# Kernel tuning notes

Measured on AMD Instinct MI355X. Metric: run time of the kernel, lower is better.

Reference implementation:

```python
import jax, jax.numpy as jnp
import numpy as np

N_USERS = 100000
M_ITEMS = 50000
N = N_USERS + M_ITEMS
D = 64
NNZ = 4800000
N_LAYERS = 3


def spmm(idx, val, x):
    # sparse COO (idx[0]=rows, idx[1]=cols) @ dense x : gather-scale-scatter
    rows, cols = idx[0], idx[1]
    return jax.ops.segment_sum(val[:, None] * x[cols], rows, num_segments=N)


def propagate(idx, val, emb0):
    # LightGCN propagation: mean over layer-0..n_layers embeddings
    embs = [emb0]
    e = emb0
    for _ in range(N_LAYERS):
        e = spmm(idx, val, e)
        embs.append(e)
    return jnp.mean(jnp.stack(embs, axis=1), axis=1)  # [N, D]


def setup_inputs() -> dict:
    key = jax.random.key(0)
    ks = jax.random.split(key, 10)
    return {
        "emb_im": 0.1 * jax.random.normal(ks[0], (N, D), jnp.float32),
        "emb_q": 0.1 * jax.random.normal(ks[1], (N, D), jnp.float32),
        "emb_p": 0.1 * jax.random.normal(ks[2], (N, D), jnp.float32),
        "g_im_idx": jax.random.randint(ks[3], (2, NNZ), 0, N, jnp.int32),
        "g_im_val": jax.random.uniform(ks[4], (NNZ,), jnp.float32) / 32.0,
        "g_q_idx": jax.random.randint(ks[5], (2, NNZ), 0, N, jnp.int32),
        "g_q_val": jax.random.uniform(ks[6], (NNZ,), jnp.float32) / 32.0,
        "g_p_idx": jax.random.randint(ks[7], (2, NNZ), 0, N, jnp.int32),
        "g_p_val": jax.random.uniform(ks[8], (NNZ,), jnp.float32) / 32.0,
        "add_weight": jnp.ones((3,), jnp.float32),
    }


def reference(emb_im, emb_q, emb_p, g_im_idx, g_im_val, g_q_idx, g_q_val,
              g_p_idx, g_p_val, add_weight):
    out_im = propagate(g_im_idx, g_im_val, emb_im)
    out_q = propagate(g_q_idx, g_q_val, emb_q)
    out_p = propagate(g_p_idx, g_p_val, emb_p)
    # weighted_add over factors: sum_f w_f * out_f ; users/items split is a
    # row split of this combined [N, D] matrix
    stacked = jnp.stack([out_im, out_q, out_p], axis=0)  # [3, N, D]
    combined = jnp.sum(stacked * add_weight[:, None, None], axis=0)  # [N, D]
    return combined  # rows [:N_USERS] = users, rows [N_USERS:] = items
```

## Files before the change

### kernel.cpp

```cpp
#include <hip/hip_runtime.h>

#define N_TOTAL 150000
#define DIM 64
#define RPB 256
#define NBUCK 586
#define CAP 9024
#define CHUNK 8192

typedef float v2f __attribute__((ext_vector_type(2)));

__global__ void fill_bcur_kernel(int* __restrict__ bcur) {
    int t = blockIdx.x * 256 + threadIdx.x;
    if (t < NBUCK) bcur[t] = t * CAP;
}

__global__ void bin_kernel(const int* __restrict__ idx, const float* __restrict__ val,
                           int* __restrict__ bcur, uint2* __restrict__ binned, int nnz) {
    __shared__ uint2 sedge[CHUNK];
    __shared__ int lcnt[NBUCK];
    __shared__ int lstart[NBUCK + 1];
    __shared__ int gbase[NBUCK];
    __shared__ int ssc[512];
    int t = threadIdx.x;
    int base = blockIdx.x * CHUNK;
    int nEdges = min(CHUNK, nnz - base);
    for (int b = t; b < NBUCK; b += 512) lcnt[b] = 0;
    __syncthreads();
    uint2 myedge[16];
    int myb[16];
    #pragma unroll
    for (int i = 0; i < 16; ++i) {
        int e = base + t + i * 512;
        if (e < nnz) {
            int r = idx[e];
            myb[i] = r >> 8;
            myedge[i].x = ((unsigned)(r & 255) << 18) | (unsigned)idx[nnz + e];
            myedge[i].y = __float_as_uint(val[e]);
            atomicAdd(&lcnt[r >> 8], 1);
        } else {
            myb[i] = -1;
        }
    }
    __syncthreads();
    int i0 = 2 * t;
    int c0 = (i0 < NBUCK) ? lcnt[i0] : 0;
    int c1 = (i0 + 1 < NBUCK) ? lcnt[i0 + 1] : 0;
    int s2 = c0 + c1;
    ssc[t] = s2;
    __syncthreads();
    for (int off = 1; off < 512; off <<= 1) {
        int x = (t >= off) ? ssc[t - off] : 0;
        __syncthreads();
        ssc[t] += x;
        __syncthreads();
    }
    int excl = ssc[t] - s2;
    if (i0 <= NBUCK) lstart[i0] = excl;
    if (i0 + 1 <= NBUCK) lstart[i0 + 1] = excl + c0;
    for (int b = t; b < NBUCK; b += 512) {
        int c = lcnt[b];
        gbase[b] = c ? atomicAdd(&bcur[b], c) : 0;
        lcnt[b] = 0;
    }
    __syncthreads();
    #pragma unroll
    for (int i = 0; i < 16; ++i) {
        int b = myb[i];
        if (b >= 0) {
            int o = atomicAdd(&lcnt[b], 1);
            sedge[lstart[b] + o] = myedge[i];
        }
    }
    __syncthreads();
    for (int p = t; p < nEdges; p += 512) {
        int lo = 0, hi = NBUCK;
        while (hi - lo > 1) {
            int mid = (lo + hi) >> 1;
            if (lstart[mid] <= p) lo = mid; else hi = mid;
        }
        int dst = gbase[lo] + (p - lstart[lo]);
        if (dst < (lo + 1) * CAP)
            binned[dst] = sedge[p];
    }
}

__global__ void scatterc_kernel(const uint2* __restrict__ binned, const int* __restrict__ bcur,
                                int* __restrict__ rlo, int* __restrict__ rhi,
                                unsigned* __restrict__ cs) {
    __shared__ int hist[RPB];
    __shared__ int cur[RPB];
    int b = blockIdx.x;
    int s = b * CAP;
    int e = min(bcur[b], s + CAP);
    int t = threadIdx.x;
    hist[t] = 0;
    __syncthreads();
    for (int k = s + t; k < e; k += 256)
        atomicAdd(&hist[binned[k].x >> 18], 1);
    __syncthreads();
    int v = hist[t];
    cur[t] = v;
    __syncthreads();
    for (int off = 1; off < 256; off <<= 1) {
        int x = (t >= off) ? cur[t - off] : 0;
        __syncthreads();
        cur[t] += x;
        __syncthreads();
    }
    int rbase = s + cur[t] - v;
    int row = (b << 8) + t;
    if (row < N_TOTAL) { rlo[row] = rbase; rhi[row] = rbase + v; }
    cur[t] = rbase;
    __syncthreads();
    for (int k = s + t; k < e; k += 256) {
        uint2 ed = binned[k];
        int rl = ed.x >> 18;
        int o = atomicAdd(&cur[rl], 1);
        unsigned v14 = (ed.y + 0x20000u) >> 18;
        cs[o] = ((ed.x & 0x3FFFFu) << 14) | v14;
    }
}

__global__ void init_out_kernel(const float* __restrict__ e0, const float* __restrict__ e1,
                                const float* __restrict__ e2, const float* __restrict__ w,
                                float* __restrict__ out, int n4) {
    int i = blockIdx.x * blockDim.x + threadIdx.x;
    if (i >= n4) return;
    float c0 = w[0] * 0.25f, c1 = w[1] * 0.25f, c2 = w[2] * 0.25f;
    float4 a = reinterpret_cast<const float4*>(e0)[i];
    float4 b = reinterpret_cast<const float4*>(e1)[i];
    float4 c = reinterpret_cast<const float4*>(e2)[i];
    float4 o;
    o.x = c0 * a.x + c1 * b.x + c2 * c.x;
    o.y = c0 * a.y + c1 * b.y + c2 * c.y;
    o.z = c0 * a.z + c1 * b.z + c2 * c.z;
    o.w = c0 * a.w + c1 * b.w + c2 * c.w;
    reinterpret_cast<float4*>(out)[i] = o;
}

__global__ void conv_fp8_kernel(const float* __restrict__ x, uint2* __restrict__ y, int n8) {
    int i = blockIdx.x * blockDim.x + threadIdx.x;
    if (i >= n8) return;
    const float4* x4 = reinterpret_cast<const float4*>(x);
    float4 a = x4[2 * i], b = x4[2 * i + 1];
    int p0 = __builtin_amdgcn_cvt_pk_fp8_f32(a.x * 64.f, a.y * 64.f, 0, false);
    p0 = __builtin_amdgcn_cvt_pk_fp8_f32(a.z * 64.f, a.w * 64.f, p0, true);
    int p1 = __builtin_amdgcn_cvt_pk_fp8_f32(b.x * 64.f, b.y * 64.f, 0, false);
    p1 = __builtin_amdgcn_cvt_pk_fp8_f32(b.z * 64.f, b.w * 64.f, p1, true);
    uint2 o;
    o.x = (unsigned)p0;
    o.y = (unsigned)p1;
    y[i] = o;
}

template <bool LAST>
__global__ void spmm_fp8_kernel(const int* __restrict__ rlo, const int* __restrict__ rhi,
                                const unsigned* __restrict__ cs, const unsigned* __restrict__ x,
                                unsigned* __restrict__ y, float* __restrict__ out,
                                const float* __restrict__ w, int f, int nrows) {
    int gid = blockIdx.x * blockDim.x + threadIdx.x;
    int row = gid >> 6;
    int lane = gid & 63;
    if (row >= nrows) return;
    int s = rlo[row], e = rhi[row];
    int q = lane >> 4, sub = lane & 15;
    float ac[4][4];
    #pragma unroll
    for (int j = 0; j < 4; ++j) {
        ac[j][0] = 0.f; ac[j][1] = 0.f; ac[j][2] = 0.f; ac[j][3] = 0.f;
    }
    int k = s + q;
    for (; k + 12 < e; k += 16) {
        unsigned ed[4], g[4];
        #pragma unroll
        for (int j = 0; j < 4; ++j) ed[j] = cs[k + 4 * j];
        #pragma unroll
        for (int j = 0; j < 4; ++j) g[j] = x[((size_t)(ed[j] >> 14) << 4) + sub];
        #pragma unroll
        for (int j = 0; j < 4; ++j) {
            float vv = __uint_as_float((ed[j] & 0x3FFFu) << 18);
            v2f lo = __builtin_amdgcn_cvt_pk_f32_fp8((int)g[j], false);
            v2f hi = __builtin_amdgcn_cvt_pk_f32_fp8((int)g[j], true);
            ac[j][0] += vv * lo.x;
            ac[j][1] += vv * lo.y;
            ac[j][2] += vv * hi.x;
            ac[j][3] += vv * hi.y;
        }
    }
    for (; k < e; k += 4) {
        unsigned ed = cs[k];
        unsigned g = x[((size_t)(ed >> 14) << 4) + sub];
        float vv = __uint_as_float((ed & 0x3FFFu) << 18);
        v2f lo = __builtin_amdgcn_cvt_pk_f32_fp8((int)g, false);
        v2f hi = __builtin_amdgcn_cvt_pk_f32_fp8((int)g, true);
        ac[0][0] += vv * lo.x;
        ac[0][1] += vv * lo.y;
        ac[0][2] += vv * hi.x;
        ac[0][3] += vv * hi.y;
    }
    float a0 = (ac[0][0] + ac[1][0]) + (ac[2][0] + ac[3][0]);
    float a1 = (ac[0][1] + ac[1][1]) + (ac[2][1] + ac[3][1]);
    float a2 = (ac[0][2] + ac[1][2]) + (ac[2][2] + ac[3][2]);
    float a3 = (ac[0][3] + ac[1][3]) + (ac[2][3] + ac[3][3]);
    a0 += __shfl_xor(a0, 16); a0 += __shfl_xor(a0, 32);
    a1 += __shfl_xor(a1, 16); a1 += __shfl_xor(a1, 32);
    a2 += __shfl_xor(a2, 16); a2 += __shfl_xor(a2, 32);
    a3 += __shfl_xor(a3, 16); a3 += __shfl_xor(a3, 32);
    if (q == 0) {
        if (!LAST) {
            int p = __builtin_amdgcn_cvt_pk_fp8_f32(a0, a1, 0, false);
            p = __builtin_amdgcn_cvt_pk_fp8_f32(a2, a3, p, true);
            y[((size_t)row << 4) + sub] = (unsigned)p;
        }
        float c = w[f] * (0.25f / 64.f);
        float4* o4 = reinterpret_cast<float4*>(out) + (((size_t)row << 4) + sub);
        float4 cv = *o4;
        cv.x += c * a0;
        cv.y += c * a1;
        cv.z += c * a2;
        cv.w += c * a3;
        *o4 = cv;
    }
}

extern "C" void kernel_launch(void* const* d_in, const int* in_sizes, int n_in,
                              void* d_out, int out_size, void* d_ws, size_t ws_size,
                              hipStream_t stream) {
    const float* emb[3]  = {(const float*)d_in[0], (const float*)d_in[1], (const float*)d_in[2]};
    const int*   gidx[3] = {(const int*)d_in[3],   (const int*)d_in[5],   (const int*)d_in[7]};
    const float* gval[3] = {(const float*)d_in[4], (const float*)d_in[6], (const float*)d_in[8]};
    const float* w = (const float*)d_in[9];
    float* out = (float*)d_out;

    const int nnz = in_sizes[4];
    const size_t bufElems = (size_t)N_TOTAL * DIM;
    const size_t fp8Bytes = bufElems;
    const size_t capElems = (size_t)NBUCK * CAP;

    char* base = (char*)d_ws;
    uint2*    binned = (uint2*)base;
    unsigned* emb8   = (unsigned*)base;
    unsigned* bufA8  = (unsigned*)(base + fp8Bytes);
    unsigned* bufB8  = (unsigned*)(base + 2 * fp8Bytes);
    unsigned* cs     = (unsigned*)(base + capElems * 8);
    int*      rlo    = (int*)(base + capElems * 8 + capElems * 4);
    int*      rhi    = rlo + N_TOTAL;
    int*      bcur   = rhi + N_TOTAL;

    const int n4 = (int)(bufElems / 4);
    const int n8 = (int)(bufElems / 8);
    dim3 eltGrid((n4 + 255) / 256);
    dim3 cvtGrid((n8 + 255) / 256);
    dim3 chunkGrid((nnz + CHUNK - 1) / CHUNK);
    dim3 rowGrid((unsigned)(((size_t)N_TOTAL * 64 + 255) / 256));

    init_out_kernel<<<eltGrid, 256, 0, stream>>>(emb[0], emb[1], emb[2], w, out, n4);

    for (int f = 0; f < 3; ++f) {
        fill_bcur_kernel<<<3, 256, 0, stream>>>(bcur);
        bin_kernel<<<chunkGrid, 512, 0, stream>>>(gidx[f], gval[f], bcur, binned, nnz);
        scatterc_kernel<<<NBUCK, 256, 0, stream>>>(binned, bcur, rlo, rhi, cs);

        conv_fp8_kernel<<<cvtGrid, 256, 0, stream>>>(emb[f], (uint2*)emb8, n8);

        spmm_fp8_kernel<false><<<rowGrid, 256, 0, stream>>>(rlo, rhi, cs, emb8, bufA8,
                                                            out, w, f, N_TOTAL);
        spmm_fp8_kernel<false><<<rowGrid, 256, 0, stream>>>(rlo, rhi, cs, bufA8, bufB8,
                                                            out, w, f, N_TOTAL);
        spmm_fp8_kernel<true><<<rowGrid, 256, 0, stream>>>(rlo, rhi, cs, bufB8, nullptr,
                                                           out, w, f, N_TOTAL);
    }
}
```

Baseline: 1.155 ms.

## Add column-sorted LDS-accumulate SpMM sweep for first factor's first layer

Rebuckets rows into 512 buckets of 293 rows using a magic-number division. For factor 0 it adds a second column-sorted copy of the edges with 16-bit local row ids. A new sweep kernel accumulates each bucket's rows in LDS with shared-memory atomics, aiming for better gather locality on x. The path depends on workspace size and uses more memory. It also adds LDS atomic contention, and float atomics make the summation order nondeterministic.

```diff
diff --git a/kernel.cpp b/kernel.cpp
--- a/kernel.cpp
+++ b/kernel.cpp
@@ -2,10 +2,12 @@
 
 #define N_TOTAL 150000
 #define DIM 64
-#define RPB 256
-#define NBUCK 586
-#define CAP 9024
+#define RPB 293
+#define NBUCK 512
+#define MAGIC 14658592u
+#define CAP 10368
 #define CHUNK 8192
+#define ASTRIDE 65
 
 typedef float v2f __attribute__((ext_vector_type(2)));
 
@@ -20,11 +22,10 @@
     __shared__ int lcnt[NBUCK];
     __shared__ int lstart[NBUCK + 1];
     __shared__ int gbase[NBUCK];
-    __shared__ int ssc[512];
     int t = threadIdx.x;
     int base = blockIdx.x * CHUNK;
     int nEdges = min(CHUNK, nnz - base);
-    for (int b = t; b < NBUCK; b += 512) lcnt[b] = 0;
+    lcnt[t] = 0;
     __syncthreads();
     uint2 myedge[16];
     int myb[16];
@@ -33,35 +34,32 @@
         int e = base + t + i * 512;
         if (e < nnz) {
             int r = idx[e];
-            myb[i] = r >> 8;
-            myedge[i].x = ((unsigned)(r & 255) << 18) | (unsigned)idx[nnz + e];
+            int b = (int)__umulhi((unsigned)r, MAGIC);
+            myb[i] = b;
+            unsigned rloc = (unsigned)(r - b * RPB);
+            myedge[i].x = (rloc << 18) | (unsigned)idx[nnz + e];
             myedge[i].y = __float_as_uint(val[e]);
-            atomicAdd(&lcnt[r >> 8], 1);
+            atomicAdd(&lcnt[b], 1);
         } else {
             myb[i] = -1;
         }
     }
     __syncthreads();
-    int i0 = 2 * t;
-    int c0 = (i0 < NBUCK) ? lcnt[i0] : 0;
-    int c1 = (i0 + 1 < NBUCK) ? lcnt[i0 + 1] : 0;
-    int s2 = c0 + c1;
-    ssc[t] = s2;
+    int c = lcnt[t];
+    lstart[t] = c;
     __syncthreads();
     for (int off = 1; off < 512; off <<= 1) {
-        int x = (t >= off) ? ssc[t - off] : 0;
-        __syncthreads();
-        ssc[t] += x;
-        __syncthreads();
-    }
-    int excl = ssc[t] - s2;
-    if (i0 <= NBUCK) lstart[i0] = excl;
-    if (i0 + 1 <= NBUCK) lstart[i0 + 1] = excl + c0;
-    for (int b = t; b < NBUCK; b += 512) {
-        int c = lcnt[b];
-        gbase[b] = c ? atomicAdd(&bcur[b], c) : 0;
-        lcnt[b] = 0;
-    }
+        int x = (t >= off) ? lstart[t - off] : 0;
+        __syncthreads();
+        lstart[t] += x;
+        __syncthreads();
+    }
+    int incl = lstart[t];
+    __syncthreads();
+    lstart[t] = incl - c;
+    if (t == 511) lstart[512] = incl;
+    gbase[t] = c ? atomicAdd(&bcur[t], c) : 0;
+    lcnt[t] = 0;
     __syncthreads();
     #pragma unroll
     for (int i = 0; i < 16; ++i) {
@@ -84,38 +82,91 @@
     }
 }
 
-__global__ void scatterc_kernel(const uint2* __restrict__ binned, const int* __restrict__ bcur,
-                                int* __restrict__ rlo, int* __restrict__ rhi,
-                                unsigned* __restrict__ cs) {
+__global__ void scatterc_col_kernel(const uint2* __restrict__ binned,
+                                    const int* __restrict__ bcur,
+                                    unsigned short* __restrict__ rl,
+                                    unsigned* __restrict__ cs) {
+    __shared__ int hist[NBUCK];
+    __shared__ int ssc[256];
+    int b = blockIdx.x, t = threadIdx.x;
+    int s = b * CAP, e = min(bcur[b], s + CAP);
+    hist[t] = 0; hist[t + 256] = 0;
+    __syncthreads();
+    for (int k = s + t; k < e; k += 256) {
+        unsigned col = binned[k].x & 0x3FFFFu;
+        atomicAdd(&hist[__umulhi(col, MAGIC)], 1);
+    }
+    __syncthreads();
+    int i0 = 2 * t;
+    int c0 = hist[i0], c1 = hist[i0 + 1];
+    int s2 = c0 + c1;
+    ssc[t] = s2;
+    __syncthreads();
+    for (int off = 1; off < 256; off <<= 1) {
+        int x = (t >= off) ? ssc[t - off] : 0;
+        __syncthreads();
+        ssc[t] += x;
+        __syncthreads();
+    }
+    int excl = ssc[t] - s2;
+    __syncthreads();
+    hist[i0] = s + excl;
+    hist[i0 + 1] = s + excl + c0;
+    __syncthreads();
+    for (int k = s + t; k < e; k += 256) {
+        uint2 ed = binned[k];
+        unsigned col = ed.x & 0x3FFFFu;
+        int cb = (int)__umulhi(col, MAGIC);
+        int o = atomicAdd(&hist[cb], 1);
+        unsigned v14 = (ed.y + 0x20000u) >> 18;
+        cs[o] = (col << 14) | v14;
+        rl[o] = (unsigned short)(ed.x >> 18);
+    }
+}
+
+__global__ void scatterc_row_kernel(const uint2* __restrict__ binned,
+                                    const int* __restrict__ bcur,
+                                    int* __restrict__ rlo, int* __restrict__ rhi,
+                                    unsigned* __restrict__ cs) {
     __shared__ int hist[RPB];
-    __shared__ int cur[RPB];
-    int b = blockIdx.x;
-    int s = b * CAP;
-    int e = min(bcur[b], s + CAP);
-    int t = threadIdx.x;
-    hist[t] = 0;
+    __shared__ int ssc[256];
+    int b = blockIdx.x, t = threadIdx.x;
+    int s = b * CAP, e = min(bcur[b], s + CAP);
+    for (int i = t; i < RPB; i += 256) hist[i] = 0;
     __syncthreads();
     for (int k = s + t; k < e; k += 256)
         atomicAdd(&hist[binned[k].x >> 18], 1);
     __syncthreads();
-    int v = hist[t];
-    cur[t] = v;
+    int i0 = 2 * t;
+    int c0 = (i0 < RPB) ? hist[i0] : 0;
+    int c1 = (i0 + 1 < RPB) ? hist[i0 + 1] : 0;
+    int s2 = c0 + c1;
+    ssc[t] = s2;
     __syncthreads();
     for (int off = 1; off < 256; off <<= 1) {
-        int x = (t >= off) ? cur[t - off] : 0;
-        __syncthreads();
-        cur[t] += x;
-        __syncthreads();
-    }
-    int rbase = s + cur[t] - v;
-    int row = (b << 8) + t;
-    if (row < N_TOTAL) { rlo[row] = rbase; rhi[row] = rbase + v; }
-    cur[t] = rbase;
+        int x = (t >= off) ? ssc[t - off] : 0;
+        __syncthreads();
+        ssc[t] += x;
+        __syncthreads();
+    }
+    int excl = ssc[t] - s2;
+    __syncthreads();
+    int base0 = s + excl, base1 = s + excl + c0;
+    if (i0 < RPB) {
+        int row = b * RPB + i0;
+        if (row < N_TOTAL) { rlo[row] = base0; rhi[row] = base0 + c0; }
+        hist[i0] = base0;
+    }
+    if (i0 + 1 < RPB) {
+        int row = b * RPB + i0 + 1;
+        if (row < N_TOTAL) { rlo[row] = base1; rhi[row] = base1 + c1; }
+        hist[i0 + 1] = base1;
+    }
     __syncthreads();
     for (int k = s + t; k < e; k += 256) {
         uint2 ed = binned[k];
-        int rl = ed.x >> 18;
-        int o = atomicAdd(&cur[rl], 1);
+        int rl_ = ed.x >> 18;
+        int o = atomicAdd(&hist[rl_], 1);
         unsigned v14 = (ed.y + 0x20000u) >> 18;
         cs[o] = ((ed.x & 0x3FFFFu) << 14) | v14;
     }
@@ -154,7 +205,7 @@
 }
 
 template <bool LAST>
-__global__ void spmm_fp8_kernel(const int* __restrict__ rlo, const int* __restrict__ rhi,
+__global__ void spmm_reg_kernel(const int* __restrict__ rlo, const int* __restrict__ rhi,
                                 const unsigned* __restrict__ cs, const unsigned* __restrict__ x,
                                 unsigned* __restrict__ y, float* __restrict__ out,
                                 const float* __restrict__ w, int f, int nrows) {
@@ -223,6 +274,53 @@
     }
 }
 
+__global__ __launch_bounds__(256)
+void spmm_sweep_kernel(const unsigned short* __restrict__ rl, const unsigned* __restrict__ cs,
+                       const int* __restrict__ bcur, const unsigned* __restrict__ x,
+                       unsigned* __restrict__ y, float* __restrict__ out,
+                       const float* __restrict__ w, int f) {
+    __shared__ float acc[RPB * ASTRIDE];
+    int b = blockIdx.x, t = threadIdx.x;
+    int s = b * CAP, e = min(bcur[b], s + CAP);
+    for (int i = t; i < RPB * ASTRIDE; i += 256) acc[i] = 0.f;
+    __syncthreads();
+    int wid = t >> 6, q = (t >> 4) & 3, sub = t & 15;
+    for (int kb = s + wid * 4 + q; kb < e; kb += 16) {
+        unsigned ed = cs[kb];
+        int r = rl[kb];
+        unsigned g = x[((size_t)(ed >> 14) << 4) + sub];
+        float vv = __uint_as_float((ed & 0x3FFFu) << 18);
+        v2f lo = __builtin_amdgcn_cvt_pk_f32_fp8((int)g, false);
+        v2f hi = __builtin_amdgcn_cvt_pk_f32_fp8((int)g, true);
+        int a = r * ASTRIDE + sub;
+        __hip_atomic_fetch_add(&acc[a],      vv * lo.x, __ATOMIC_RELAXED, __HIP_MEMORY_SCOPE_WORKGROUP);
+        __hip_atomic_fetch_add(&acc[a + 16], vv * lo.y, __ATOMIC_RELAXED, __HIP_MEMORY_SCOPE_WORKGROUP);
+        __hip_atomic_fetch_add(&acc[a + 32], vv * hi.x, __ATOMIC_RELAXED, __HIP_MEMORY_SCOPE_WORKGROUP);
+        __hip_atomic_fetch_add(&acc[a + 48], vv * hi.y, __ATOMIC_RELAXED, __HIP_MEMORY_SCOPE_WORKGROUP);
+    }
+    __syncthreads();
+    float c = w[f] * (0.25f / 64.f);
+    int wd = t & 15;
+    for (int rr = (t >> 4); rr < RPB; rr += 16) {
+        int row = b * RPB + rr;
+        if (row >= N_TOTAL) break;
+        float a0 = acc[rr * ASTRIDE + wd];
+        float a1 = acc[rr * ASTRIDE + wd + 16];
+        float a2 = acc[rr * ASTRIDE + wd + 32];
+        float a3 = acc[rr * ASTRIDE + wd + 48];
+        int p = __builtin_amdgcn_cvt_pk_fp8_f32(a0, a1, 0, false);
+        p = __builtin_amdgcn_cvt_pk_fp8_f32(a2, a3, p, true);
+        y[((size_t)row << 4) + wd] = (unsigned)p;
+        float4* o4 = reinterpret_cast<float4*>(out) + (((size_t)row << 4) + wd);
+        float4 cv = *o4;
+        cv.x += c * a0;
+        cv.y += c * a1;
+        cv.z += c * a2;
+        cv.w += c * a3;
+        *o4 = cv;
+    }
+}
+
 extern "C" void kernel_launch(void* const* d_in, const int* in_sizes, int n_in,
                               void* d_out, int out_size, void* d_ws, size_t ws_size,
                               hipStream_t stream) {
@@ -238,14 +336,21 @@
     const size_t capElems = (size_t)NBUCK * CAP;
 
     char* base = (char*)d_ws;
-    uint2*    binned = (uint2*)base;
-    unsigned* emb8   = (unsigned*)base;
-    unsigned* bufA8  = (unsigned*)(base + fp8Bytes);
-    unsigned* bufB8  = (unsigned*)(base + 2 * fp8Bytes);
-    unsigned* cs     = (unsigned*)(base + capElems * 8);
-    int*      rlo    = (int*)(base + capElems * 8 + capElems * 4);
-    int*      rhi    = rlo + N_TOTAL;
-    int*      bcur   = rhi + N_TOTAL;
+    uint2*          binned = (uint2*)base;
+    unsigned*       emb8   = (unsigned*)base;
+    unsigned*       bufA8  = (unsigned*)(base + fp8Bytes);
+    unsigned*       bufB8  = (unsigned*)(base + 2 * fp8Bytes);
+    unsigned*       cs     = (unsigned*)(base + capElems * 8);
+    unsigned short* rl     = (unsigned short*)(base + capElems * 8 + capElems * 4);
+    int*            rlo12  = (int*)rl;
+    int*            rhi12  = rlo12 + N_TOTAL;
+    int*            bcur   = (int*)(base + capElems * 14);
+    unsigned*       csr0   = (unsigned*)((char*)bcur + 4096);
+    int*            f0rlo  = (int*)(csr0 + capElems);
+    int*            f0rhi  = f0rlo + N_TOTAL;
+    const size_t needHybrid = capElems * 14 + 4096 + capElems * 4
+                            + (size_t)2 * N_TOTAL * 4;
+    const bool hybrid = ws_size >= needHybrid;
 
     const int n4 = (int)(bufElems / 4);
     const int n8 = (int)(bufElems / 8);
@@ -257,17 +362,27 @@
     init_out_kernel<<<eltGrid, 256, 0, stream>>>(emb[0], emb[1], emb[2], w, out, n4);
 
     for (int f = 0; f < 3; ++f) {
-        fill_bcur_kernel<<<3, 256, 0, stream>>>(bcur);
+        fill_bcur_kernel<<<2, 256, 0, stream>>>(bcur);
         bin_kernel<<<chunkGrid, 512, 0, stream>>>(gidx[f], gval[f], bcur, binned, nnz);
-        scatterc_kernel<<<NBUCK, 256, 0, stream>>>(binned, bcur, rlo, rhi, cs);
-
-        conv_fp8_kernel<<<cvtGrid, 256, 0, stream>>>(emb[f], (uint2*)emb8, n8);
-
-        spmm_fp8_kernel<false><<<rowGrid, 256, 0, stream>>>(rlo, rhi, cs, emb8, bufA8,
-                                                            out, w, f, N_TOTAL);
-        spmm_fp8_kernel<false><<<rowGrid, 256, 0, stream>>>(rlo, rhi, cs, bufA8, bufB8,
-                                                            out, w, f, N_TOTAL);
-        spmm_fp8_kernel<true><<<rowGrid, 256, 0, stream>>>(rlo, rhi, cs, bufB8, nullptr,
-                                                           out, w, f, N_TOTAL);
-    }
-}
+
+        if (f == 0 && hybrid) {
+            scatterc_col_kernel<<<NBUCK, 256, 0, stream>>>(binned, bcur, rl, cs);
+            scatterc_row_kernel<<<NBUCK, 256, 0, stream>>>(binned, bcur, f0rlo, f0rhi, csr0);
+            conv_fp8_kernel<<<cvtGrid, 256, 0, stream>>>(emb[0], (uint2*)emb8, n8);
+            spmm_sweep_kernel<<<NBUCK, 256, 0, stream>>>(rl, cs, bcur, emb8, bufA8, out, w, 0);
+            spmm_reg_kernel<false><<<rowGrid, 256, 0, stream>>>(f0rlo, f0rhi, csr0, bufA8, bufB8,
+                                                                out, w, 0, N_TOTAL);
+            spmm_reg_kernel<true><<<rowGrid, 256, 0, stream>>>(f0rlo, f0rhi, csr0, bufB8, nullptr,
+                                                               out, w, 0, N_TOTAL);
+        } else {
+            scatterc_row_kernel<<<NBUCK, 256, 0, stream>>>(binned, bcur, rlo12, rhi12, cs);
+            conv_fp8_kernel<<<cvtGrid, 256, 0, stream>>>(emb[f], (uint2*)emb8, n8);
+            spmm_reg_kernel<false><<<rowGrid, 256, 0, stream>>>(rlo12, rhi12, cs, emb8, bufA8,
+                                                                out, w, f, N_TOTAL);
+            spmm_reg_kernel<false><<<rowGrid, 256, 0, stream>>>(rlo12, rhi12, cs, bufA8, bufB8,
+                                                                out, w, f, N_TOTAL);
+            spmm_reg_kernel<true><<<rowGrid, 256, 0, stream>>>(rlo12, rhi12, cs, bufB8, nullptr,
+                                                               out, w, f, N_TOTAL);
+        }
+    }
+}
```

New measurement: 2.688 ms. 2.33x slower.

## Move output accumulation to per-factor combine kernel and use 512 non-pow2 row buckets

Applied to the files above, without the earlier changes.

The per-layer read-modify-write of the fp32 output inside each SpMM is removed. SpMM now only writes fp8 layer results, and a single combine kernel per factor reads the embedding and the three fp8 layers and accumulates into the output, which also replaces the init kernel. Row binning switches from 586 buckets of 256 rows to 512 buckets of 293 rows, using a magic-multiply divide, so the bin kernel's prefix scan runs one bucket per thread. The scatter kernel adapts its scan to handle two rows per thread. The last layer now gets an extra fp8 round trip through memory, and the output is built from fp8-quantized layers in a different order.

```diff
diff --git a/kernel.cpp b/kernel.cpp
--- a/kernel.cpp
+++ b/kernel.cpp
@@ -2,9 +2,10 @@
 
 #define N_TOTAL 150000
 #define DIM 64
-#define RPB 256
-#define NBUCK 586
-#define CAP 9024
+#define RPB 293
+#define NBUCK 512
+#define MAGIC 14658592u
+#define CAP 10368
 #define CHUNK 8192
 
 typedef float v2f __attribute__((ext_vector_type(2)));
@@ -20,11 +21,10 @@
     __shared__ int lcnt[NBUCK];
     __shared__ int lstart[NBUCK + 1];
     __shared__ int gbase[NBUCK];
-    __shared__ int ssc[512];
     int t = threadIdx.x;
     int base = blockIdx.x * CHUNK;
     int nEdges = min(CHUNK, nnz - base);
-    for (int b = t; b < NBUCK; b += 512) lcnt[b] = 0;
+    lcnt[t] = 0;
     __syncthreads();
     uint2 myedge[16];
     int myb[16];
@@ -33,35 +33,32 @@
         int e = base + t + i * 512;
         if (e < nnz) {
             int r = idx[e];
-            myb[i] = r >> 8;
-            myedge[i].x = ((unsigned)(r & 255) << 18) | (unsigned)idx[nnz + e];
+            int b = (int)__umulhi((unsigned)r, MAGIC);
+            myb[i] = b;
+            unsigned rloc = (unsigned)(r - b * RPB);
+            myedge[i].x = (rloc << 18) | (unsigned)idx[nnz + e];
             myedge[i].y = __float_as_uint(val[e]);
-            atomicAdd(&lcnt[r >> 8], 1);
+            atomicAdd(&lcnt[b], 1);
         } else {
             myb[i] = -1;
         }
     }
     __syncthreads();
-    int i0 = 2 * t;
-    int c0 = (i0 < NBUCK) ? lcnt[i0] : 0;
-    int c1 = (i0 + 1 < NBUCK) ? lcnt[i0 + 1] : 0;
-    int s2 = c0 + c1;
-    ssc[t] = s2;
+    int c = lcnt[t];
+    lstart[t] = c;
     __syncthreads();
     for (int off = 1; off < 512; off <<= 1) {
-        int x = (t >= off) ? ssc[t - off] : 0;
-        __syncthreads();
-        ssc[t] += x;
-        __syncthreads();
-    }
-    int excl = ssc[t] - s2;
-    if (i0 <= NBUCK) lstart[i0] = excl;
-    if (i0 + 1 <= NBUCK) lstart[i0 + 1] = excl + c0;
-    for (int b = t; b < NBUCK; b += 512) {
-        int c = lcnt[b];
-        gbase[b] = c ? atomicAdd(&bcur[b], c) : 0;
-        lcnt[b] = 0;
-    }
+        int x = (t >= off) ? lstart[t - off] : 0;
+        __syncthreads();
+        lstart[t] += x;
+        __syncthreads();
+    }
+    int incl = lstart[t];
+    __syncthreads();
+    lstart[t] = incl - c;
+    if (t == 511) lstart[512] = incl;
+    gbase[t] = c ? atomicAdd(&bcur[t], c) : 0;
+    lcnt[t] = 0;
     __syncthreads();
     #pragma unroll
     for (int i = 0; i < 16; ++i) {
@@ -84,58 +81,52 @@
     }
 }
 
-__global__ void scatterc_kernel(const uint2* __restrict__ binned, const int* __restrict__ bcur,
+__global__ void scatterc_kernel(const uint2* __restrict__ binned,
+                                const int* __restrict__ bcur,
                                 int* __restrict__ rlo, int* __restrict__ rhi,
                                 unsigned* __restrict__ cs) {
     __shared__ int hist[RPB];
-    __shared__ int cur[RPB];
-    int b = blockIdx.x;
-    int s = b * CAP;
-    int e = min(bcur[b], s + CAP);
-    int t = threadIdx.x;
-    hist[t] = 0;
+    __shared__ int ssc[256];
+    int b = blockIdx.x, t = threadIdx.x;
+    int s = b * CAP, e = min(bcur[b], s + CAP);
+    for (int i = t; i < RPB; i += 256) hist[i] = 0;
     __syncthreads();
     for (int k = s + t; k < e; k += 256)
         atomicAdd(&hist[binned[k].x >> 18], 1);
     __syncthreads();
-    int v = hist[t];
-    cur[t] = v;
+    int i0 = 2 * t;
+    int c0 = (i0 < RPB) ? hist[i0] : 0;
+    int c1 = (i0 + 1 < RPB) ? hist[i0 + 1] : 0;
+    int s2 = c0 + c1;
+    ssc[t] = s2;
     __syncthreads();
     for (int off = 1; off < 256; off <<= 1) {
-        int x = (t >= off) ? cur[t - off] : 0;
-        __syncthreads();
-        cur[t] += x;
-        __syncthreads();
-    }
-    int rbase = s + cur[t] - v;
-    int row = (b << 8) + t;
-    if (row < N_TOTAL) { rlo[row] = rbase; rhi[row] = rbase + v; }
-    cur[t] = rbase;
+        int x = (t >= off) ? ssc[t - off] : 0;
+        __syncthreads();
+        ssc[t] += x;
+        __syncthreads();
+    }
+    int excl = ssc[t] - s2;
+    __syncthreads();
+    int base0 = s + excl, base1 = s + excl + c0;
+    if (i0 < RPB) {
+        int row = b * RPB + i0;
+        if (row < N_TOTAL) { rlo[row] = base0; rhi[row] = base0 + c0; }
+        hist[i0] = base0;
+    }
+    if (i0 + 1 < RPB) {
+        int row = b * RPB + i0 + 1;
+        if (row < N_TOTAL) { rlo[row] = base1; rhi[row] = base1 + c1; }
+        hist[i0 + 1] = base1;
+    }
     __syncthreads();
     for (int k = s + t; k < e; k += 256) {
         uint2 ed = binned[k];
-        int rl = ed.x >> 18;
-        int o = atomicAdd(&cur[rl], 1);
+        int rl_ = ed.x >> 18;
+        int o = atomicAdd(&hist[rl_], 1);
         unsigned v14 = (ed.y + 0x20000u) >> 18;
         cs[o] = ((ed.x & 0x3FFFFu) << 14) | v14;
     }
-}
-
-__global__ void init_out_kernel(const float* __restrict__ e0, const float* __restrict__ e1,
-                                const float* __restrict__ e2, const float* __restrict__ w,
-                                float* __restrict__ out, int n4) {
-    int i = blockIdx.x * blockDim.x + threadIdx.x;
-    if (i >= n4) return;
-    float c0 = w[0] * 0.25f, c1 = w[1] * 0.25f, c2 = w[2] * 0.25f;
-    float4 a = reinterpret_cast<const float4*>(e0)[i];
-    float4 b = reinterpret_cast<const float4*>(e1)[i];
-    float4 c = reinterpret_cast<const float4*>(e2)[i];
-    float4 o;
-    o.x = c0 * a.x + c1 * b.x + c2 * c.x;
-    o.y = c0 * a.y + c1 * b.y + c2 * c.y;
-    o.z = c0 * a.z + c1 * b.z + c2 * c.z;
-    o.w = c0 * a.w + c1 * b.w + c2 * c.w;
-    reinterpret_cast<float4*>(out)[i] = o;
 }
 
 __global__ void conv_fp8_kernel(const float* __restrict__ x, uint2* __restrict__ y, int n8) {
@@ -153,11 +144,9 @@
     y[i] = o;
 }
 
-template <bool LAST>
 __global__ void spmm_fp8_kernel(const int* __restrict__ rlo, const int* __restrict__ rhi,
                                 const unsigned* __restrict__ cs, const unsigned* __restrict__ x,
-                                unsigned* __restrict__ y, float* __restrict__ out,
-                                const float* __restrict__ w, int f, int nrows) {
+                                unsigned* __restrict__ y, int nrows) {
     int gid = blockIdx.x * blockDim.x + threadIdx.x;
     int row = gid >> 6;
     int lane = gid & 63;
@@ -207,18 +196,40 @@
     a2 += __shfl_xor(a2, 16); a2 += __shfl_xor(a2, 32);
     a3 += __shfl_xor(a3, 16); a3 += __shfl_xor(a3, 32);
     if (q == 0) {
-        if (!LAST) {
-            int p = __builtin_amdgcn_cvt_pk_fp8_f32(a0, a1, 0, false);
-            p = __builtin_amdgcn_cvt_pk_fp8_f32(a2, a3, p, true);
-            y[((size_t)row << 4) + sub] = (unsigned)p;
-        }
-        float c = w[f] * (0.25f / 64.f);
-        float4* o4 = reinterpret_cast<float4*>(out) + (((size_t)row << 4) + sub);
+        int p = __builtin_amdgcn_cvt_pk_fp8_f32(a0, a1, 0, false);
+        p = __builtin_amdgcn_cvt_pk_fp8_f32(a2, a3, p, true);
+        y[((size_t)row << 4) + sub] = (unsigned)p;
+    }
+}
+
+template <bool FIRST>
+__global__ void combine_kernel(const float* __restrict__ emb, const unsigned* __restrict__ A,
+                               const unsigned* __restrict__ B, const unsigned* __restrict__ C,
+                               const float* __restrict__ w, int f, float* __restrict__ out,
+                               int nwords) {
+    int i = blockIdx.x * blockDim.x + threadIdx.x;
+    if (i >= nwords) return;
+    float c = w[f] * 0.25f;
+    const float kInv = 1.f / 64.f;
+    float4 e = reinterpret_cast<const float4*>(emb)[i];
+    unsigned a = A[i], b = B[i], cc = C[i];
+    v2f alo = __builtin_amdgcn_cvt_pk_f32_fp8((int)a, false);
+    v2f ahi = __builtin_amdgcn_cvt_pk_f32_fp8((int)a, true);
+    v2f blo = __builtin_amdgcn_cvt_pk_f32_fp8((int)b, false);
+    v2f bhi = __builtin_amdgcn_cvt_pk_f32_fp8((int)b, true);
+    v2f clo = __builtin_amdgcn_cvt_pk_f32_fp8((int)cc, false);
+    v2f chi = __builtin_amdgcn_cvt_pk_f32_fp8((int)cc, true);
+    float4 o;
+    o.x = c * (e.x + (alo.x + blo.x + clo.x) * kInv);
+    o.y = c * (e.y + (alo.y + blo.y + clo.y) * kInv);
+    o.z = c * (e.z + (ahi.x + bhi.x + chi.x) * kInv);
+    o.w = c * (e.w + (ahi.y + bhi.y + chi.y) * kInv);
+    float4* o4 = reinterpret_cast<float4*>(out) + i;
+    if (FIRST) {
+        *o4 = o;
+    } else {
         float4 cv = *o4;
-        cv.x += c * a0;
-        cv.y += c * a1;
-        cv.z += c * a2;
-        cv.w += c * a3;
+        cv.x += o.x; cv.y += o.y; cv.z += o.z; cv.w += o.w;
         *o4 = cv;
     }
 }
@@ -240,34 +251,37 @@
     char* base = (char*)d_ws;
     uint2*    binned = (uint2*)base;
     unsigned* emb8   = (unsigned*)base;
-    unsigned* bufA8  = (unsigned*)(base + fp8Bytes);
-    unsigned* bufB8  = (unsigned*)(base + 2 * fp8Bytes);
+    unsigned* A8     = (unsigned*)(base + fp8Bytes);
+    unsigned* B8     = (unsigned*)(base + 2 * fp8Bytes);
+    unsigned* C8     = (unsigned*)(base + 3 * fp8Bytes);
     unsigned* cs     = (unsigned*)(base + capElems * 8);
     int*      rlo    = (int*)(base + capElems * 8 + capElems * 4);
     int*      rhi    = rlo + N_TOTAL;
     int*      bcur   = rhi + N_TOTAL;
 
-    const int n4 = (int)(bufElems / 4);
     const int n8 = (int)(bufElems / 8);
-    dim3 eltGrid((n4 + 255) / 256);
+    const int nwords = (int)(bufElems / 4);
     dim3 cvtGrid((n8 + 255) / 256);
+    dim3 cmbGrid((nwords + 255) / 256);
     dim3 chunkGrid((nnz + CHUNK - 1) / CHUNK);
     dim3 rowGrid((unsigned)(((size_t)N_TOTAL * 64 + 255) / 256));
 
-    init_out_kernel<<<eltGrid, 256, 0, stream>>>(emb[0], emb[1], emb[2], w, out, n4);
-
     for (int f = 0; f < 3; ++f) {
-        fill_bcur_kernel<<<3, 256, 0, stream>>>(bcur);
+        fill_bcur_kernel<<<2, 256, 0, stream>>>(bcur);
         bin_kernel<<<chunkGrid, 512, 0, stream>>>(gidx[f], gval[f], bcur, binned, nnz);
         scatterc_kernel<<<NBUCK, 256, 0, stream>>>(binned, bcur, rlo, rhi, cs);
 
         conv_fp8_kernel<<<cvtGrid, 256, 0, stream>>>(emb[f], (uint2*)emb8, n8);
 
-        spmm_fp8_kernel<false><<<rowGrid, 256, 0, stream>>>(rlo, rhi, cs, emb8, bufA8,
-                                                            out, w, f, N_TOTAL);
-        spmm_fp8_kernel<false><<<rowGrid, 256, 0, stream>>>(rlo, rhi, cs, bufA8, bufB8,
-                                                            out, w, f, N_TOTAL);
-        spmm_fp8_kernel<true><<<rowGrid, 256, 0, stream>>>(rlo, rhi, cs, bufB8, nullptr,
-                                                           out, w, f, N_TOTAL);
-    }
-}
+        spmm_fp8_kernel<<<rowGrid, 256, 0, stream>>>(rlo, rhi, cs, emb8, A8, N_TOTAL);
+        spmm_fp8_kernel<<<rowGrid, 256, 0, stream>>>(rlo, rhi, cs, A8, B8, N_TOTAL);
+        spmm_fp8_kernel<<<rowGrid, 256, 0, stream>>>(rlo, rhi, cs, B8, C8, N_TOTAL);
+
+        if (f == 0)
+            combine_kernel<true><<<cmbGrid, 256, 0, stream>>>(emb[f], A8, B8, C8, w, f,
+                                                              out, nwords);
+        else
+            combine_kernel<false><<<cmbGrid, 256, 0, stream>>>(emb[f], A8, B8, C8, w, f,
+                                                               out, nwords);
+    }
+}
```

New measurement: 1.093 ms. 5.3% less time.
